# Performance work log

Measured on AMD Instinct MI355X. Metric: run time of the kernel, lower is better.

## Reference

```python
import jax, jax.numpy as jnp
import numpy as np
import math

EMB = 128
N_HEADS = 8
HEAD_DIM = EMB // N_HEADS
TANH_CLIP = 10.0
NEG_INF = -1e9


def make_heads(x, n_heads):
    # x: (B, n, H) -> (B, n_heads, n, head_dim)
    B, n, H = x.shape
    return x.reshape(B, n, n_heads, H // n_heads).transpose(0, 2, 1, 3)


def setup_inputs() -> dict:
    key = jax.random.key(0)
    ks = jax.random.split(key, 11)
    B, N, H = 64, 2000, EMB
    s = 1.0 / math.sqrt(H)
    return {
        "patch_embeddings": jax.random.normal(ks[0], (B, N, H), jnp.float32),
        "fixed_content_cls": jax.random.normal(ks[1], (B, 1, H), jnp.float32),
        "Wq_graph": jax.random.normal(ks[2], (H, H), jnp.float32) * s,
        "Wq_first": jax.random.normal(ks[3], (H, H), jnp.float32) * s,
        "Wq_last": jax.random.normal(ks[4], (H, H), jnp.float32) * s,
        "Wk": jax.random.normal(ks[5], (H, H), jnp.float32) * s,
        "Wv": jax.random.normal(ks[6], (H, H), jnp.float32) * s,
        "logit_Wk": jax.random.normal(ks[7], (H, H), jnp.float32) * s,
        "Wc": jax.random.normal(ks[8], (H, H), jnp.float32) * s,
        "bc": jax.random.normal(ks[9], (H,), jnp.float32) * s,
        "last_patch": jax.random.randint(ks[10], (B,), 0, N, jnp.int64),
    }


def reference(patch_embeddings, fixed_content_cls, Wq_graph, Wq_first, Wq_last,
              Wk, Wv, logit_Wk, Wc, bc, last_patch):
    B, N, H = patch_embeddings.shape
    bidx = jnp.arange(B)

    # reset(): precomputed projections over all patches (memory-dominant)
    q_graph = make_heads(fixed_content_cls @ Wq_graph.T, N_HEADS)   # (B, nh, 1, hd)
    glimpse_k = make_heads(patch_embeddings @ Wk.T, N_HEADS)        # (B, nh, N, hd)
    glimpse_v = make_heads(patch_embeddings @ Wv.T, N_HEADS)        # (B, nh, N, hd)
    logit_k = patch_embeddings @ logit_Wk.T                          # (B, N, H)

    # mask the just-visited patch (emulate -inf with large negative for stability)
    mask = jnp.zeros((B, N), patch_embeddings.dtype).at[bidx, last_patch].set(NEG_INF)

    # gather last patch embedding: (B, 1, H)
    last_emb = patch_embeddings[bidx, last_patch][:, None, :]
    q_first = make_heads(last_emb @ Wq_first.T, N_HEADS)
    q_last = make_heads(last_emb @ Wq_last.T, N_HEADS)
    glimpse_q = q_graph + q_first + q_last                          # (B, nh, 1, hd)

    # masked multi-head attention, q_len = 1
    scores = jnp.einsum('bhqd,bhnd->bhqn', glimpse_q, glimpse_k) / math.sqrt(HEAD_DIM)
    scores = scores + mask[:, None, None, :]
    attn = jax.nn.softmax(scores, axis=-1)
    out = jnp.einsum('bhqn,bhnd->bhqd', attn, glimpse_v)            # (B, nh, 1, hd)
    out = out.transpose(0, 2, 1, 3).reshape(B, 1, H)

    final_q = out @ Wc.T + bc                                        # (B, 1, H)

    # tanh-clipped pointer logits over all N patches
    score = jnp.einsum('bqh,bnh->bqn', final_q, logit_k) / math.sqrt(H)  # (B, 1, N)
    score_masked = TANH_CLIP * jnp.tanh(score[:, 0, :]) + mask          # (B, N)
    probs = jax.nn.softmax(score_masked, axis=1)
    return probs
```

## Files before the change

kernel.cpp:

```cpp
#include <hip/hip_runtime.h>
#include <hip/hip_cooperative_groups.h>
#include <math.h>

namespace cg = cooperative_groups;

#define BB 64
#define NN 2000
#define HH 128
#define NHEAD 8
#define SP 8
#define RPB 250

#define SM_BYTES 24528


__device__ __forceinline__ void body_qk(
    const float* pe, const float* cls, const float* Wqg, const float* Wqf,
    const float* Wql, const float* Wk, int b, int last, int tid,
    float4* sc4, float4* sl4, float* qv, float* qk) {
  if (tid < 32) {
    sc4[tid] = ((const float4*)(cls + b*HH))[tid];
    sl4[tid] = ((const float4*)(pe + ((long)b*NN + last)*HH))[tid];
  }
  __syncthreads();
  if (tid < 128) {
    const float4* wg = (const float4*)(Wqg + tid*HH);
    const float4* wf = (const float4*)(Wqf + tid*HH);
    const float4* wl = (const float4*)(Wql + tid*HH);
    float acc = 0.f;
    #pragma unroll 8
    for (int j = 0; j < 32; j++) {
      float4 g = wg[j], f = wf[j], l = wl[j], c = sc4[j], s = sl4[j];
      acc += g.x*c.x + g.y*c.y + g.z*c.z + g.w*c.w;
      acc += (f.x+l.x)*s.x + (f.y+l.y)*s.y + (f.z+l.z)*s.z + (f.w+l.w)*s.w;
    }
    qv[tid] = acc;
  }
  __syncthreads();
  if (tid < 128) {
    #pragma unroll
    for (int h = 0; h < NHEAD; h++) {
      float a = 0.f;
      #pragma unroll
      for (int d = 0; d < 16; d++)
        a += qv[h*16+d] * Wk[(h*16+d)*HH + tid];
      qk[(b*NHEAD + h)*HH + tid] = a * 0.25f;
    }
  }
}

__device__ __forceinline__ void body_scores_wsum(
    const float* pe, const float* qk, int b, int sp, int last, int tid,
    float (*pl)[NHEAD], float4 (*wred)[4][32], float (*lred)[NHEAD],
    float* Wpart, float* lpart) {
  const int n0 = sp * RPB;
  if (tid < RPB) {
    const int n = n0 + tid;
    const float4* prow = (const float4*)(pe + ((long)b*NN + n)*HH);
    const float4* qk4  = (const float4*)(qk + (long)b*NHEAD*HH);
    float d[NHEAD];
    #pragma unroll
    for (int h = 0; h < NHEAD; h++) d[h] = 0.f;
    #pragma unroll 2
    for (int j = 0; j < 32; j += 4) {
      float4 v0 = prow[j], v1 = prow[j+1], v2 = prow[j+2], v3 = prow[j+3];
      #pragma unroll
      for (int h = 0; h < NHEAD; h++) {
        float4 q0 = qk4[h*32+j],   q1 = qk4[h*32+j+1];
        float4 q2 = qk4[h*32+j+2], q3 = qk4[h*32+j+3];
        d[h] += v0.x*q0.x + v0.y*q0.y + v0.z*q0.z + v0.w*q0.w
              + v1.x*q1.x + v1.y*q1.y + v1.z*q1.z + v1.w*q1.w
              + v2.x*q2.x + v2.y*q2.y + v2.z*q2.z + v2.w*q2.w
              + v3.x*q3.x + v3.y*q3.y + v3.z*q3.z + v3.w*q3.w;
      }
    }
    const bool live = (n != last);
    float4 p0, p1;
    p0.x = live ? __expf(d[0]) : 0.f;  p0.y = live ? __expf(d[1]) : 0.f;
    p0.z = live ? __expf(d[2]) : 0.f;  p0.w = live ? __expf(d[3]) : 0.f;
    p1.x = live ? __expf(d[4]) : 0.f;  p1.y = live ? __expf(d[5]) : 0.f;
    p1.z = live ? __expf(d[6]) : 0.f;  p1.w = live ? __expf(d[7]) : 0.f;
    ((float4*)pl[tid])[0] = p0;
    ((float4*)pl[tid])[1] = p1;
  }
  __syncthreads();

  const int w = tid >> 6, lane = tid & 63;
  const int st = w*2 + (lane >> 5);
  const int j4 = lane & 31;
  const float4* peg = (const float4*)(pe + ((long)b*NN + n0)*HH);
  float4 wa[NHEAD];
  float  la[NHEAD];
  #pragma unroll
  for (int h = 0; h < NHEAD; h++) { wa[h] = make_float4(0.f,0.f,0.f,0.f); la[h] = 0.f; }
  #pragma unroll 4
  for (int i = 0; i < 32; i++) {
    const int nl = st + (i << 3);
    if (nl < RPB) {
      float4 v  = peg[nl*32 + j4];
      float4 pa = *(const float4*)&pl[nl][0];
      float4 pb = *(const float4*)&pl[nl][4];
      wa[0].x += pa.x*v.x; wa[0].y += pa.x*v.y; wa[0].z += pa.x*v.z; wa[0].w += pa.x*v.w; la[0] += pa.x;
      wa[1].x += pa.y*v.x; wa[1].y += pa.y*v.y; wa[1].z += pa.y*v.z; wa[1].w += pa.y*v.w; la[1] += pa.y;
      wa[2].x += pa.z*v.x; wa[2].y += pa.z*v.y; wa[2].z += pa.z*v.z; wa[2].w += pa.z*v.w; la[2] += pa.z;
      wa[3].x += pa.w*v.x; wa[3].y += pa.w*v.y; wa[3].z += pa.w*v.z; wa[3].w += pa.w*v.w; la[3] += pa.w;
      wa[4].x += pb.x*v.x; wa[4].y += pb.x*v.y; wa[4].z += pb.x*v.z; wa[4].w += pb.x*v.w; la[4] += pb.x;
      wa[5].x += pb.y*v.x; wa[5].y += pb.y*v.y; wa[5].z += pb.y*v.z; wa[5].w += pb.y*v.w; la[5] += pb.y;
      wa[6].x += pb.z*v.x; wa[6].y += pb.z*v.y; wa[6].z += pb.z*v.z; wa[6].w += pb.z*v.w; la[6] += pb.z;
      wa[7].x += pb.w*v.x; wa[7].y += pb.w*v.y; wa[7].z += pb.w*v.z; wa[7].w += pb.w*v.w; la[7] += pb.w;
    }
  }
  #pragma unroll
  for (int h = 0; h < NHEAD; h++) {
    wa[h].x += __shfl_xor(wa[h].x, 32);
    wa[h].y += __shfl_xor(wa[h].y, 32);
    wa[h].z += __shfl_xor(wa[h].z, 32);
    wa[h].w += __shfl_xor(wa[h].w, 32);
    la[h]   += __shfl_xor(la[h], 32);
  }
  if (lane < 32) {
    #pragma unroll
    for (int h = 0; h < NHEAD; h++) wred[h][w][lane] = wa[h];
  }
  if (lane == 0) {
    #pragma unroll
    for (int h = 0; h < NHEAD; h++) lred[w][h] = la[h];
  }
  __syncthreads();
  const int h2 = tid >> 5, c = tid & 31;
  float4 s0 = wred[h2][0][c], s1 = wred[h2][1][c], s2 = wred[h2][2][c], s3 = wred[h2][3][c];
  float4 s;
  s.x = s0.x + s1.x + s2.x + s3.x;
  s.y = s0.y + s1.y + s2.y + s3.y;
  s.z = s0.z + s1.z + s2.z + s3.z;
  s.w = s0.w + s1.w + s2.w + s3.w;
  ((float4*)(Wpart + ((long)(b*SP + sp)*NHEAD + h2)*HH))[c] = s;
  if (tid < NHEAD)
    lpart[(b*SP + sp)*NHEAD + tid] =
        lred[0][tid] + lred[1][tid] + lred[2][tid] + lred[3][tid];
}

__device__ __forceinline__ void body_k34(
    const float* lpart, const float* Wpart, const float* Wv, const float* Wc,
    const float* bc, const float* lWk, int B2, int tid,
    float* Wns, float* lsm, float (*tmp)[HH], float* outf, float* fq,
    float* lq) {
  for (int e = tid; e < NHEAD*HH; e += 256) {
    float a = 0.f;
    #pragma unroll
    for (int s = 0; s < SP; s++) a += Wpart[((long)(B2*SP+s)*NHEAD)*HH + e];
    Wns[e] = a;
  }
  if (tid < NHEAD) {
    float l = 0.f;
    #pragma unroll
    for (int s = 0; s < SP; s++) l += lpart[(B2*SP+s)*NHEAD + tid];
    lsm[tid] = l;
  }
  __syncthreads();
  const int t = tid & 127, half = tid >> 7;
  {
    const int h = t >> 4;
    const float4* wv = (const float4*)(Wv + t*HH);
    const float4* wn = (const float4*)(Wns + h*HH);
    float a = 0.f;
    #pragma unroll 4
    for (int j = half*16; j < half*16 + 16; j++) {
      float4 v = wv[j], nn = wn[j];
      a += v.x*nn.x + v.y*nn.y + v.z*nn.z + v.w*nn.w;
    }
    tmp[half][t] = a;
    __syncthreads();
    if (half == 0) outf[t] = (tmp[0][t] + tmp[1][t]) / lsm[t>>4];
    __syncthreads();
  }
  {
    const float4* wc = (const float4*)(Wc + t*HH);
    const float4* of = (const float4*)outf;
    float a = 0.f;
    #pragma unroll 4
    for (int k = half*16; k < half*16 + 16; k++) {
      float4 v = wc[k], nn = of[k];
      a += v.x*nn.x + v.y*nn.y + v.z*nn.z + v.w*nn.w;
    }
    tmp[half][t] = a;
    __syncthreads();
    if (half == 0) fq[t] = tmp[0][t] + tmp[1][t] + bc[t];
    __syncthreads();
  }
  {
    float a = 0.f;
    #pragma unroll 4
    for (int i = half*64; i < half*64 + 64; i++)
      a += fq[i] * lWk[i*HH + t];
    tmp[half][t] = a;
    __syncthreads();
    if (half == 0)
      lq[B2*HH + t] = (tmp[0][t] + tmp[1][t]) * 0.08838834764831845f;
  }
}

__device__ __forceinline__ float body_logit(
    const float* pe, const float* lq, int b, int n, int last) {
  const float4* prow = (const float4*)(pe + ((long)b*NN + n)*HH);
  const float4* lq4  = (const float4*)(lq + (long)b*HH);
  float a0 = 0.f, a1 = 0.f, a2 = 0.f, a3 = 0.f;
  #pragma unroll 2
  for (int j = 0; j < 32; j += 4) {
    float4 v0 = prow[j], v1 = prow[j+1], v2 = prow[j+2], v3 = prow[j+3];
    float4 q0 = lq4[j], q1 = lq4[j+1], q2 = lq4[j+2], q3 = lq4[j+3];
    a0 += v0.x*q0.x + v0.y*q0.y + v0.z*q0.z + v0.w*q0.w;
    a1 += v1.x*q1.x + v1.y*q1.y + v1.z*q1.z + v1.w*q1.w;
    a2 += v2.x*q2.x + v2.y*q2.y + v2.z*q2.z + v2.w*q2.w;
    a3 += v3.x*q3.x + v3.y*q3.y + v3.z*q3.z + v3.w*q3.w;
  }
  const float acc = (a0 + a1) + (a2 + a3);
  return (n != last) ? __expf(-20.f / (__expf(2.f*acc) + 1.f)) : 0.f;
}


__global__ __launch_bounds__(256, 2) void mega(
    const float* __restrict__ pe, const float* __restrict__ cls,
    const float* __restrict__ Wqg, const float* __restrict__ Wqf,
    const float* __restrict__ Wql, const float* __restrict__ Wk,
    const float* __restrict__ Wv, const float* __restrict__ lWk,
    const float* __restrict__ Wc, const float* __restrict__ bc,
    const int* __restrict__ lp, float* __restrict__ out,
    float* __restrict__ qk, float* __restrict__ Wpart,
    float* __restrict__ lpart, float* __restrict__ lq,
    float* __restrict__ psum) {
  cg::grid_group grid = cg::this_grid();
  const int gb = blockIdx.x;
  const int b = gb >> 3, sp = gb & 7;
  const int tid = threadIdx.x;

  __shared__ __align__(16) char smraw[SM_BYTES];
  float  (*pl)[NHEAD]      = reinterpret_cast<float(*)[NHEAD]>(smraw);
  float4 (*wred)[4][32]    = reinterpret_cast<float4(*)[4][32]>(smraw + 8000);
  float  (*lred)[NHEAD]    = reinterpret_cast<float(*)[NHEAD]>(smraw + 24384);
  float4 *sc4              = reinterpret_cast<float4*>(smraw);
  float4 *sl4              = reinterpret_cast<float4*>(smraw + 512);
  float  *qv               = reinterpret_cast<float*>(smraw + 1024);
  float  *Wns              = reinterpret_cast<float*>(smraw);
  float  *lsm              = reinterpret_cast<float*>(smraw + 4096);
  float  (*tmp)[HH]        = reinterpret_cast<float(*)[HH]>(smraw + 4128);
  float  *outf             = reinterpret_cast<float*>(smraw + 5152);
  float  *fq               = reinterpret_cast<float*>(smraw + 5664);
  float  *red              = reinterpret_cast<float*>(smraw + 24512);

  const int last = lp[b];

  if (sp == 0)
    body_qk(pe, cls, Wqg, Wqf, Wql, Wk, b, last, tid, sc4, sl4, qv, qk);
  grid.sync();

  body_scores_wsum(pe, qk, b, sp, last, tid, pl, wred, lred, Wpart, lpart);
  grid.sync();

  if (gb < BB)
    body_k34(lpart, Wpart, Wv, Wc, bc, lWk, gb, tid, Wns, lsm, tmp, outf, fq, lq);
  grid.sync();

  const int n3 = sp*RPB + tid;
  float e = (tid < RPB) ? body_logit(pe, lq, b, n3, last) : 0.f;
  {
    float s = e;
    #pragma unroll
    for (int d = 1; d < 64; d <<= 1) s += __shfl_xor(s, d);
    if ((tid & 63) == 0) red[tid >> 6] = s;
    __syncthreads();
    if (tid == 0) psum[b*SP + sp] = red[0] + red[1] + red[2] + red[3];
  }
  grid.sync();

  if (tid < RPB) {
    float S = 0.f;
    #pragma unroll
    for (int s = 0; s < SP; s++) S += psum[b*SP + s];
    out[b*NN + n3] = e / S;
  }
}


__global__ __launch_bounds__(256) void fb_k1(
    const float* __restrict__ pe, const float* __restrict__ cls,
    const float* __restrict__ Wqg, const float* __restrict__ Wqf,
    const float* __restrict__ Wql, const float* __restrict__ Wk,
    const int* __restrict__ lp, float* __restrict__ qk) {
  __shared__ float4 sc4[32], sl4[32];
  __shared__ float qv[HH];
  int b = blockIdx.x;
  body_qk(pe, cls, Wqg, Wqf, Wql, Wk, b, lp[b], threadIdx.x, sc4, sl4, qv, qk);
}

__global__ __launch_bounds__(256) void fb_kb(
    const float* __restrict__ pe, const float* __restrict__ qk,
    const int* __restrict__ lp, float* __restrict__ Wpart,
    float* __restrict__ lpart) {
  __shared__ float  pl[RPB][NHEAD];
  __shared__ float4 wred[NHEAD][4][32];
  __shared__ float  lred[4][NHEAD];
  int b = blockIdx.y, sp = blockIdx.x;
  body_scores_wsum(pe, qk, b, sp, lp[b], threadIdx.x, pl, wred, lred, Wpart, lpart);
}

__global__ __launch_bounds__(256) void fb_k34(
    const float* __restrict__ lpart, const float* __restrict__ Wpart,
    const float* __restrict__ Wv, const float* __restrict__ Wc,
    const float* __restrict__ bc, const float* __restrict__ lWk,
    float* __restrict__ lq) {
  __shared__ float Wns[NHEAD*HH];
  __shared__ float lsm[NHEAD];
  __shared__ float tmp[2][HH];
  __shared__ float outf[HH], fq[HH];
  body_k34(lpart, Wpart, Wv, Wc, bc, lWk, blockIdx.x, threadIdx.x,
           Wns, lsm, tmp, outf, fq, lq);
}

__global__ __launch_bounds__(256) void fb_kd(
    const float* __restrict__ pe, const float* __restrict__ lq,
    const int* __restrict__ lp, float* __restrict__ eout,
    float* __restrict__ psum) {
  __shared__ float red[4];
  int b = blockIdx.y, sp = blockIdx.x, tid = threadIdx.x;
  int n = sp*RPB + tid;
  float e = (tid < RPB) ? body_logit(pe, lq, b, n, lp[b]) : 0.f;
  if (tid < RPB) eout[b*NN + n] = e;
  float s = e;
  #pragma unroll
  for (int d = 1; d < 64; d <<= 1) s += __shfl_xor(s, d);
  if ((tid & 63) == 0) red[tid >> 6] = s;
  __syncthreads();
  if (tid == 0) psum[b*SP + sp] = red[0] + red[1] + red[2] + red[3];
}

__global__ __launch_bounds__(256) void fb_ke(
    const float* __restrict__ eout, const float* __restrict__ psum,
    float* __restrict__ out) {
  int b = blockIdx.y, sp = blockIdx.x, tid = threadIdx.x;
  __shared__ float S;
  if (tid == 0) {
    float a = 0.f;
    #pragma unroll
    for (int s = 0; s < SP; s++) a += psum[b*SP + s];
    S = a;
  }
  __syncthreads();
  int n = sp*RPB + tid;
  if (tid < RPB) out[b*NN + n] = eout[b*NN + n] / S;
}


extern "C" void kernel_launch(void* const* d_in, const int* in_sizes, int n_in,
                              void* d_out, int out_size, void* d_ws, size_t ws_size,
                              hipStream_t stream) {
  (void)in_sizes; (void)n_in; (void)out_size; (void)ws_size;
  const float* pe   = (const float*)d_in[0];
  const float* cls  = (const float*)d_in[1];
  const float* Wqg  = (const float*)d_in[2];
  const float* Wqf  = (const float*)d_in[3];
  const float* Wql  = (const float*)d_in[4];
  const float* Wk   = (const float*)d_in[5];
  const float* Wv   = (const float*)d_in[6];
  const float* lWk  = (const float*)d_in[7];
  const float* Wc   = (const float*)d_in[8];
  const float* bc   = (const float*)d_in[9];
  const int*   lp   = (const int*)d_in[10];
  float* out = (float*)d_out;
  float* ws  = (float*)d_ws;

  float* qk    = ws;
  float* Wpart = qk + BB*NHEAD*HH;
  float* lpart = Wpart + (size_t)BB*SP*NHEAD*HH;
  float* lq    = lpart + BB*SP*NHEAD;
  float* psum  = lq + BB*HH;
  float* eout  = psum + BB*SP;

  bool coop_ok = false;
  {
    int dev = 0;
    if (hipGetDevice(&dev) == hipSuccess) {
      int attr = 0, ncu = 0, nb = 0;
      hipDeviceGetAttribute(&attr, hipDeviceAttributeCooperativeLaunch, dev);
      hipDeviceGetAttribute(&ncu, hipDeviceAttributeMultiprocessorCount, dev);
      hipError_t oe = hipOccupancyMaxActiveBlocksPerMultiprocessor(
          &nb, (const void*)mega, 256, 0);
      if (attr && oe == hipSuccess && (long)nb * ncu >= (long)BB*SP)
        coop_ok = true;
    }
  }

  if (coop_ok) {
    void* args[] = {
      (void*)&pe, (void*)&cls, (void*)&Wqg, (void*)&Wqf, (void*)&Wql,
      (void*)&Wk, (void*)&Wv, (void*)&lWk, (void*)&Wc, (void*)&bc,
      (void*)&lp, (void*)&out, (void*)&qk, (void*)&Wpart, (void*)&lpart,
      (void*)&lq, (void*)&psum
    };
    hipError_t le = hipLaunchCooperativeKernel((const void*)mega, dim3(BB*SP),
                                               dim3(256), args, 0, stream);
    if (le == hipSuccess) return;
  }

  fb_k1<<<dim3(BB), dim3(256), 0, stream>>>(pe, cls, Wqg, Wqf, Wql, Wk, lp, qk);
  fb_kb<<<dim3(SP, BB), dim3(256), 0, stream>>>(pe, qk, lp, Wpart, lpart);
  fb_k34<<<dim3(BB), dim3(256), 0, stream>>>(lpart, Wpart, Wv, Wc, bc, lWk, lq);
  fb_kd<<<dim3(SP, BB), dim3(256), 0, stream>>>(pe, lq, lp, eout, psum);
  fb_ke<<<dim3(SP, BB), dim3(256), 0, stream>>>(eout, psum, out);
}
```

Measured before the change: 73.01 us.

## Split query stage into separate kernel and recompute k34 per block to drop grid syncs

The query-projection stage moves out of the cooperative kernel into its own small launch with 128 threads, which removes the first grid-wide sync. Every block now recomputes the per-batch final-query projection redundantly and keeps it in LDS instead of writing it to global memory, which removes a second grid sync. The cost is one extra kernel launch plus eight times the small matrix-vector work per batch element, in exchange for fewer grid-wide barriers.

```diff
diff --git a/kernel.cpp b/kernel.cpp
--- a/kernel.cpp
+++ b/kernel.cpp
@@ -50,7 +50,7 @@
 }
 
 __device__ __forceinline__ void body_scores_wsum(
-    const float* pe, const float* qk, int b, int sp, int last, int tid,
+    const float* pe, const float* __restrict__ qk, int b, int sp, int last, int tid,
     float (*pl)[NHEAD], float4 (*wred)[4][32], float (*lred)[NHEAD],
     float* Wpart, float* lpart) {
   const int n0 = sp * RPB;
@@ -144,7 +144,7 @@
     const float* lpart, const float* Wpart, const float* Wv, const float* Wc,
     const float* bc, const float* lWk, int B2, int tid,
     float* Wns, float* lsm, float (*tmp)[HH], float* outf, float* fq,
-    float* lq) {
+    float* lq_dest) {
   for (int e = tid; e < NHEAD*HH; e += 256) {
     float a = 0.f;
     #pragma unroll
@@ -196,14 +196,14 @@
     tmp[half][t] = a;
     __syncthreads();
     if (half == 0)
-      lq[B2*HH + t] = (tmp[0][t] + tmp[1][t]) * 0.08838834764831845f;
+      lq_dest[t] = (tmp[0][t] + tmp[1][t]) * 0.08838834764831845f;
   }
 }
 
 __device__ __forceinline__ float body_logit(
-    const float* pe, const float* lq, int b, int n, int last) {
+    const float* pe, const float* lqp, int b, int n, int last) {
   const float4* prow = (const float4*)(pe + ((long)b*NN + n)*HH);
-  const float4* lq4  = (const float4*)(lq + (long)b*HH);
+  const float4* lq4  = (const float4*)lqp;
   float a0 = 0.f, a1 = 0.f, a2 = 0.f, a3 = 0.f;
   #pragma unroll 2
   for (int j = 0; j < 32; j += 4) {
@@ -219,70 +219,7 @@
 }
 
 
-__global__ __launch_bounds__(256, 2) void mega(
-    const float* __restrict__ pe, const float* __restrict__ cls,
-    const float* __restrict__ Wqg, const float* __restrict__ Wqf,
-    const float* __restrict__ Wql, const float* __restrict__ Wk,
-    const float* __restrict__ Wv, const float* __restrict__ lWk,
-    const float* __restrict__ Wc, const float* __restrict__ bc,
-    const int* __restrict__ lp, float* __restrict__ out,
-    float* __restrict__ qk, float* __restrict__ Wpart,
-    float* __restrict__ lpart, float* __restrict__ lq,
-    float* __restrict__ psum) {
-  cg::grid_group grid = cg::this_grid();
-  const int gb = blockIdx.x;
-  const int b = gb >> 3, sp = gb & 7;
-  const int tid = threadIdx.x;
-
-  __shared__ __align__(16) char smraw[SM_BYTES];
-  float  (*pl)[NHEAD]      = reinterpret_cast<float(*)[NHEAD]>(smraw);
-  float4 (*wred)[4][32]    = reinterpret_cast<float4(*)[4][32]>(smraw + 8000);
-  float  (*lred)[NHEAD]    = reinterpret_cast<float(*)[NHEAD]>(smraw + 24384);
-  float4 *sc4              = reinterpret_cast<float4*>(smraw);
-  float4 *sl4              = reinterpret_cast<float4*>(smraw + 512);
-  float  *qv               = reinterpret_cast<float*>(smraw + 1024);
-  float  *Wns              = reinterpret_cast<float*>(smraw);
-  float  *lsm              = reinterpret_cast<float*>(smraw + 4096);
-  float  (*tmp)[HH]        = reinterpret_cast<float(*)[HH]>(smraw + 4128);
-  float  *outf             = reinterpret_cast<float*>(smraw + 5152);
-  float  *fq               = reinterpret_cast<float*>(smraw + 5664);
-  float  *red              = reinterpret_cast<float*>(smraw + 24512);
-
-  const int last = lp[b];
-
-  if (sp == 0)
-    body_qk(pe, cls, Wqg, Wqf, Wql, Wk, b, last, tid, sc4, sl4, qv, qk);
-  grid.sync();
-
-  body_scores_wsum(pe, qk, b, sp, last, tid, pl, wred, lred, Wpart, lpart);
-  grid.sync();
-
-  if (gb < BB)
-    body_k34(lpart, Wpart, Wv, Wc, bc, lWk, gb, tid, Wns, lsm, tmp, outf, fq, lq);
-  grid.sync();
-
-  const int n3 = sp*RPB + tid;
-  float e = (tid < RPB) ? body_logit(pe, lq, b, n3, last) : 0.f;
-  {
-    float s = e;
-    #pragma unroll
-    for (int d = 1; d < 64; d <<= 1) s += __shfl_xor(s, d);
-    if ((tid & 63) == 0) red[tid >> 6] = s;
-    __syncthreads();
-    if (tid == 0) psum[b*SP + sp] = red[0] + red[1] + red[2] + red[3];
-  }
-  grid.sync();
-
-  if (tid < RPB) {
-    float S = 0.f;
-    #pragma unroll
-    for (int s = 0; s < SP; s++) S += psum[b*SP + s];
-    out[b*NN + n3] = e / S;
-  }
-}
-
-
-__global__ __launch_bounds__(256) void fb_k1(
+__global__ __launch_bounds__(128) void k1(
     const float* __restrict__ pe, const float* __restrict__ cls,
     const float* __restrict__ Wqg, const float* __restrict__ Wqf,
     const float* __restrict__ Wql, const float* __restrict__ Wk,
@@ -292,6 +229,60 @@
   int b = blockIdx.x;
   body_qk(pe, cls, Wqg, Wqf, Wql, Wk, b, lp[b], threadIdx.x, sc4, sl4, qv, qk);
 }
+
+
+__global__ __launch_bounds__(256, 2) void mega(
+    const float* __restrict__ pe, const float* __restrict__ qk,
+    const float* __restrict__ Wv, const float* __restrict__ lWk,
+    const float* __restrict__ Wc, const float* __restrict__ bc,
+    const int* __restrict__ lp, float* __restrict__ out,
+    float* __restrict__ Wpart, float* __restrict__ lpart,
+    float* __restrict__ psum) {
+  cg::grid_group grid = cg::this_grid();
+  const int gb = blockIdx.x;
+  const int b = gb >> 3, sp = gb & 7;
+  const int tid = threadIdx.x;
+
+  __shared__ __align__(16) char smraw[SM_BYTES];
+  float  (*pl)[NHEAD]   = reinterpret_cast<float(*)[NHEAD]>(smraw);
+  float4 (*wred)[4][32] = reinterpret_cast<float4(*)[4][32]>(smraw + 8000);
+  float  (*lred)[NHEAD] = reinterpret_cast<float(*)[NHEAD]>(smraw + 24384);
+  float  *Wns           = reinterpret_cast<float*>(smraw);
+  float  *lsm           = reinterpret_cast<float*>(smraw + 4096);
+  float  (*tmp)[HH]     = reinterpret_cast<float(*)[HH]>(smraw + 4128);
+  float  *outf          = reinterpret_cast<float*>(smraw + 5152);
+  float  *fq            = reinterpret_cast<float*>(smraw + 5664);
+  float  *lq_lds        = reinterpret_cast<float*>(smraw + 23296);
+  float  *red           = reinterpret_cast<float*>(smraw + 24512);
+
+  const int last = lp[b];
+
+  body_scores_wsum(pe, qk, b, sp, last, tid, pl, wred, lred, Wpart, lpart);
+  grid.sync();
+
+  body_k34(lpart, Wpart, Wv, Wc, bc, lWk, b, tid, Wns, lsm, tmp, outf, fq, lq_lds);
+  __syncthreads();
+
+  const int n3 = sp*RPB + tid;
+  float e = (tid < RPB) ? body_logit(pe, lq_lds, b, n3, last) : 0.f;
+  {
+    float s = e;
+    #pragma unroll
+    for (int d = 1; d < 64; d <<= 1) s += __shfl_xor(s, d);
+    if ((tid & 63) == 0) red[tid >> 6] = s;
+    __syncthreads();
+    if (tid == 0) psum[b*SP + sp] = red[0] + red[1] + red[2] + red[3];
+  }
+  grid.sync();
+
+  if (tid < RPB) {
+    float S = 0.f;
+    #pragma unroll
+    for (int s = 0; s < SP; s++) S += psum[b*SP + s];
+    out[b*NN + n3] = e / S;
+  }
+}
+
 
 __global__ __launch_bounds__(256) void fb_kb(
     const float* __restrict__ pe, const float* __restrict__ qk,
@@ -314,7 +305,7 @@
   __shared__ float tmp[2][HH];
   __shared__ float outf[HH], fq[HH];
   body_k34(lpart, Wpart, Wv, Wc, bc, lWk, blockIdx.x, threadIdx.x,
-           Wns, lsm, tmp, outf, fq, lq);
+           Wns, lsm, tmp, outf, fq, lq + blockIdx.x*HH);
 }
 
 __global__ __launch_bounds__(256) void fb_kd(
@@ -324,7 +315,7 @@
   __shared__ float red[4];
   int b = blockIdx.y, sp = blockIdx.x, tid = threadIdx.x;
   int n = sp*RPB + tid;
-  float e = (tid < RPB) ? body_logit(pe, lq, b, n, lp[b]) : 0.f;
+  float e = (tid < RPB) ? body_logit(pe, lq + (long)b*HH, b, n, lp[b]) : 0.f;
   if (tid < RPB) eout[b*NN + n] = e;
   float s = e;
   #pragma unroll
@@ -390,19 +381,18 @@
     }
   }
 
+  k1<<<dim3(BB), dim3(128), 0, stream>>>(pe, cls, Wqg, Wqf, Wql, Wk, lp, qk);
+
   if (coop_ok) {
     void* args[] = {
-      (void*)&pe, (void*)&cls, (void*)&Wqg, (void*)&Wqf, (void*)&Wql,
-      (void*)&Wk, (void*)&Wv, (void*)&lWk, (void*)&Wc, (void*)&bc,
-      (void*)&lp, (void*)&out, (void*)&qk, (void*)&Wpart, (void*)&lpart,
-      (void*)&lq, (void*)&psum
+      (void*)&pe, (void*)&qk, (void*)&Wv, (void*)&lWk, (void*)&Wc, (void*)&bc,
+      (void*)&lp, (void*)&out, (void*)&Wpart, (void*)&lpart, (void*)&psum
     };
     hipError_t le = hipLaunchCooperativeKernel((const void*)mega, dim3(BB*SP),
                                                dim3(256), args, 0, stream);
     if (le == hipSuccess) return;
   }
 
-  fb_k1<<<dim3(BB), dim3(256), 0, stream>>>(pe, cls, Wqg, Wqf, Wql, Wk, lp, qk);
   fb_kb<<<dim3(SP, BB), dim3(256), 0, stream>>>(pe, qk, lp, Wpart, lpart);
   fb_k34<<<dim3(BB), dim3(256), 0, stream>>>(lpart, Wpart, Wv, Wc, bc, lWk, lq);
   fb_kd<<<dim3(SP, BB), dim3(256), 0, stream>>>(pe, lq, lp, eout, psum);
```

Result: no change. 73.11 us (+0.1%).
